# Optimization experiments

Hardware: AMD Instinct MI355X
Metric: run time of the kernel (lower is better)

## Reference

```python
import jax, jax.numpy as jnp
import numpy as np

GROUPS = 32
HEADS = 8
EPS = 1e-5


def setup_inputs() -> dict:
    key = jax.random.key(0)
    k1, k2 = jax.random.split(key)
    B, C, H, W = 8, 512, 32, 32
    x = jax.random.normal(k1, (B, C, H, W), dtype=jnp.float32)
    gn_weight = jnp.ones((C,), dtype=jnp.float32)
    gn_bias = jnp.zeros((C,), dtype=jnp.float32)
    w1 = jax.random.normal(k2, (3 * C, C, 1), dtype=jnp.float32) * (C ** -0.5)
    b1 = jnp.zeros((3 * C,), dtype=jnp.float32)
    return {"x": x, "gn_weight": gn_weight, "gn_bias": gn_bias, "w1": w1, "b1": b1}


def reference(x, gn_weight, gn_bias, w1, b1):
    B, C, H, W = x.shape
    T = H * W
    ch = C // HEADS
    # GroupNorm over (C/G, H, W) per group
    xg = x.reshape(B, GROUPS, -1)
    mu = jnp.mean(xg, axis=-1, keepdims=True)
    var = jnp.var(xg, axis=-1, keepdims=True)
    xn = ((xg - mu) * jax.lax.rsqrt(var + EPS)).reshape(B, C, T)
    xn = xn * gn_weight[:, None] + gn_bias[:, None]
    # 1x1 Conv1d -> QKV: [B, 3C, T]
    qkv = jnp.einsum('oc,bct->bot', w1[:, :, 0], xn) + b1[:, None]
    q, k, v = jnp.split(qkv, 3, axis=1)
    q = q.reshape(B, HEADS, ch, T)
    k = k.reshape(B, HEADS, ch, T)
    v = v.reshape(B, HEADS, ch, T)
    scale = ch ** -0.25  # applied to both q and k, per guided-diffusion QKVAttention
    w = jnp.einsum('bhct,bhcs->bhts', q * scale, k * scale)  # [B,H,T,T]
    w = jax.nn.softmax(w, axis=-1)
    a = jnp.einsum('bhts,bhcs->bhct', w, v).reshape(B, C, H, W)
    return a + x
```

## Files before the change

### kernel.cpp

```cpp
#include <hip/hip_runtime.h>
#include <hip/hip_bf16.h>

#define NB 8
#define NC 512
#define NT 1024
#define NHEADS 8
#define NCH 64
#define NGROUPS 32
#define NGC 16

typedef __attribute__((ext_vector_type(4))) unsigned short u16x4;
typedef __attribute__((ext_vector_type(8))) unsigned short u16x8;
typedef __attribute__((ext_vector_type(4))) float f32x4;
typedef __attribute__((ext_vector_type(8))) __bf16 bfv8;

static __device__ __forceinline__ unsigned short f2bf(float f) {
    __bf16 h = (__bf16)f;
    return __builtin_bit_cast(unsigned short, h);
}

static __device__ __forceinline__ f32x4 mfma_bf16(u16x8 a, u16x8 b, f32x4 c) {
    return __builtin_amdgcn_mfma_f32_16x16x32_bf16(
        __builtin_bit_cast(bfv8, a), __builtin_bit_cast(bfv8, b), c, 0, 0, 0);
}

static __device__ __forceinline__ void gl_lds16(const unsigned short* g, unsigned short* l) {
    __builtin_amdgcn_global_load_lds(
        (const __attribute__((address_space(1))) unsigned int*)g,
        (__attribute__((address_space(3))) unsigned int*)l, 16, 0, 0);
}

__global__ __launch_bounds__(512) void k_gn_w1(const float* __restrict__ x,
                                               const float* __restrict__ gw,
                                               const float* __restrict__ gb,
                                               const float* __restrict__ w1,
                                               unsigned short* __restrict__ xnT,
                                               unsigned short* __restrict__ w1b) {
    int tid = threadIdx.x;
    if (blockIdx.x >= 256) {
        int i = ((blockIdx.x - 256) * 512 + tid) * 8;
        f32x4 a = *(const f32x4*)(w1 + i);
        f32x4 b = *(const f32x4*)(w1 + i + 4);
        u16x8 o;
#pragma unroll
        for (int j = 0; j < 4; ++j) { o[j] = f2bf(a[j]); o[4 + j] = f2bf(b[j]); }
        *(u16x8*)(w1b + i) = o;
        return;
    }
    int b = blockIdx.x >> 5, g = blockIdx.x & 31;
    int half = tid >> 8, tl = tid & 255;
    int t4 = tl * 4;
    const float* xb = x + ((size_t)(b * NC + g * NGC + half * 8)) * NT;

    f32x4 vv[8];
    float s = 0.f, ss = 0.f;
#pragma unroll
    for (int cc = 0; cc < 8; ++cc) {
        f32x4 v = *(const f32x4*)(xb + cc * NT + t4);
        vv[cc] = v;
#pragma unroll
        for (int i = 0; i < 4; ++i) { s += v[i]; ss += v[i] * v[i]; }
    }
#pragma unroll
    for (int off = 1; off < 64; off <<= 1) { s += __shfl_xor(s, off); ss += __shfl_xor(ss, off); }
    __shared__ float rs_[8], rss[8];
    int w = tid >> 6;
    if ((tid & 63) == 0) { rs_[w] = s; rss[w] = ss; }
    __syncthreads();
    s = 0.f; ss = 0.f;
#pragma unroll
    for (int i = 0; i < 8; ++i) { s += rs_[i]; ss += rss[i]; }
    float mu  = s * (1.f / 16384.f);
    float var = ss * (1.f / 16384.f) - mu * mu;
    float rstd = rsqrtf(var + 1e-5f);

    float wgt[8], bia[8];
#pragma unroll
    for (int cc = 0; cc < 8; ++cc) {
        float ww = gw[g * NGC + half * 8 + cc] * rstd;
        wgt[cc] = ww;
        bia[cc] = gb[g * NGC + half * 8 + cc] - mu * ww;
    }
#pragma unroll
    for (int i = 0; i < 4; ++i) {
        unsigned short o[8];
#pragma unroll
        for (int cc = 0; cc < 8; ++cc) o[cc] = f2bf(vv[cc][i] * wgt[cc] + bia[cc]);
        unsigned short* dst = xnT + ((size_t)(b * NT + t4 + i)) * NC + g * NGC + half * 8;
        *(u16x8*)dst = *(u16x8*)o;
    }
}

__global__ __launch_bounds__(256) void k_qkv_gemm(const unsigned short* __restrict__ w1b,
                                                  const unsigned short* __restrict__ xnT,
                                                  const float* __restrict__ b1,
                                                  unsigned short* __restrict__ q_t,
                                                  unsigned short* __restrict__ k_t,
                                                  unsigned short* __restrict__ vbuf) {
    __shared__ unsigned short As[2 * 128 * 64];
    __shared__ unsigned short Bs[2 * 128 * 64];
    int bid = blockIdx.x;
    int lbid = (bid & 7) * 96 + (bid >> 3);
    int bb = lbid / 96;
    int rr_ = lbid % 96;
    int tm = rr_ >> 3, tn = rr_ & 7;
    int tid = threadIdx.x;
    int l = tid & 63, w = tid >> 6;
    int wm = w >> 1, wn = w & 1;
    int ll = l & 15, lg = l >> 4;
    int rl = l >> 3, sl = l & 7;
    int ssl = sl ^ rl;

    const unsigned short* Ag = w1b + (size_t)(tm * 128) * NC;
    const unsigned short* Bg = xnT + (size_t)(bb * NT + tn * 128) * NC;

    auto STAGE = [&](int k0, int buf) {
        unsigned short* dA = As + buf * 8192 + w * 32 * 64;
        unsigned short* dB = Bs + buf * 8192 + w * 32 * 64;
#pragma unroll
        for (int i = 0; i < 4; ++i) {
            int row = w * 32 + i * 8 + rl;
            gl_lds16(Ag + (size_t)row * NC + k0 + ssl * 8, dA + i * 512);
            gl_lds16(Bg + (size_t)row * NC + k0 + ssl * 8, dB + i * 512);
        }
    };

    f32x4 acc[4][4] = {};
    STAGE(0, 0);
    __syncthreads();
    int cur = 0;
    for (int ks = 0; ks < 8; ++ks) {
        if (ks < 7) STAGE((ks + 1) * 64, cur ^ 1);
        const char* Ac = (const char*)(As + cur * 8192);
        const char* Bc = (const char*)(Bs + cur * 8192);
#pragma unroll
        for (int kk = 0; kk < 2; ++kk) {
            u16x8 af[4], bf[4];
#pragma unroll
            for (int m = 0; m < 4; ++m) {
                int row = wm * 64 + m * 16 + ll;
                af[m] = *(const u16x8*)(Ac + row * 128 + ((kk * 64 + lg * 16) ^ ((row & 7) << 4)));
            }
#pragma unroll
            for (int n = 0; n < 4; ++n) {
                int row = wn * 64 + n * 16 + ll;
                bf[n] = *(const u16x8*)(Bc + row * 128 + ((kk * 64 + lg * 16) ^ ((row & 7) << 4)));
            }
#pragma unroll
            for (int m = 0; m < 4; ++m)
#pragma unroll
                for (int n = 0; n < 4; ++n)
                    acc[m][n] = mfma_bf16(af[m], bf[n], acc[m][n]);
        }
        __syncthreads();
        cur ^= 1;
    }

    if (tm < 8) {
        int qk = tm >> 2;
        int h = (tm & 3) * 2 + wm;
        float sc = qk ? 1.f : 0.125f * 1.44269504088896f;
        int obase = tm * 128 + wm * 64;
        unsigned short* dst = (qk ? k_t : q_t) + ((size_t)(bb * 8 + h)) * NT * NCH;
#pragma unroll
        for (int m = 0; m < 4; ++m) {
#pragma unroll
            for (int n = 0; n < 4; ++n) {
                int t = tn * 128 + wn * 64 + n * 16 + ll;
                u16x4 pk;
#pragma unroll
                for (int r = 0; r < 4; ++r)
                    pk[r] = f2bf((acc[m][n][r] + b1[obase + m * 16 + lg * 4 + r]) * sc);
                *(u16x4*)(dst + (size_t)t * NCH + m * 16 + lg * 4) = pk;
            }
        }
    } else {
        int vcb = (tm - 8) * 128 + wm * 64;
#pragma unroll
        for (int m = 0; m < 4; ++m)
#pragma unroll
            for (int r = 0; r < 4; ++r) {
                int vc = vcb + m * 16 + lg * 4 + r;
                float bias = b1[1024 + vc];
#pragma unroll
                for (int n = 0; n < 4; ++n) {
                    int t = tn * 128 + wn * 64 + n * 16 + ll;
                    vbuf[(size_t)(bb * NC + vc) * NT + t] = f2bf(acc[m][n][r] + bias);
                }
            }
    }
}

#define SW1B(r) (((r) & 7) << 4)
__global__ __launch_bounds__(256) void k_attn(const unsigned short* __restrict__ q_t,
                                              const unsigned short* __restrict__ k_t,
                                              const unsigned short* __restrict__ vbuf,
                                              const float* __restrict__ x,
                                              float* __restrict__ out) {
    __shared__ unsigned char smem[49152];
    unsigned short* sK = (unsigned short*)smem;
    unsigned short* sV = (unsigned short*)(smem + 16384);
    unsigned short* sP = (unsigned short*)(smem + 32768);

    int lbid = ((blockIdx.x & 7) << 6) | (blockIdx.x >> 3);
    int b  = lbid >> 6;
    int h  = (lbid >> 3) & 7;
    int qt = lbid & 7;
    int t0 = qt * 128;

    int tid = threadIdx.x;
    int l = tid & 63, w = tid >> 6;
    int ll = l & 15, lg = l >> 4;
    int rl = l >> 3, sl = l & 7;
    int ssl = sl ^ rl;

    const unsigned short* Qg = q_t + ((size_t)((b * 8 + h) * NT + t0 + w * 32)) * NCH;
    const unsigned short* Kg = k_t + ((size_t)(b * 8 + h)) * NT * NCH;
    const unsigned short* Vg = vbuf + ((size_t)(b * NC + h * NCH)) * NT;

    u16x8 aq[2][2];
#pragma unroll
    for (int m = 0; m < 2; ++m)
#pragma unroll
        for (int kk = 0; kk < 2; ++kk)
            aq[m][kk] = *(const u16x8*)(Qg + (m * 16 + ll) * NCH + kk * 32 + lg * 8);

    f32x4 acc_o[2][4] = {};
    float rs[2] = {};

    auto STAGE = [&](int s0, int buf) {
        unsigned short* dK = sK + buf * 4096 + w * 1024;
        unsigned short* dV = sV + buf * 4096 + w * 1024;
#pragma unroll
        for (int i = 0; i < 2; ++i) {
            int row = w * 16 + i * 8 + rl;
            gl_lds16(Kg + (size_t)(s0 + row) * NCH + ssl * 8, dK + i * 512);
            gl_lds16(Vg + (size_t)row * NT + s0 + ssl * 8, dV + i * 512);
        }
    };

    STAGE(0, 0);
    __syncthreads();

    char* sPw = (char*)(sP + w * 2048);
    int cur = 0;
    for (int tile = 0; tile < 16; ++tile) {
        if (tile < 15) STAGE((tile + 1) * 64, cur ^ 1);
        const char* Kc = (const char*)(sK + cur * 4096);
        const char* Vc = (const char*)(sV + cur * 4096);

        f32x4 sc_[2][4];
#pragma unroll
        for (int j = 0; j < 4; ++j) {
            int row = j * 16 + ll;
            int sw = SW1B(row);
            u16x8 b0 = *(const u16x8*)(Kc + row * 128 + ((lg * 16) ^ sw));
            u16x8 b1v = *(const u16x8*)(Kc + row * 128 + ((64 + lg * 16) ^ sw));
            f32x4 z = {0.f, 0.f, 0.f, 0.f};
            sc_[0][j] = mfma_bf16(b1v, aq[0][1], mfma_bf16(b0, aq[0][0], z));
            sc_[1][j] = mfma_bf16(b1v, aq[1][1], mfma_bf16(b0, aq[1][0], z));
        }

#pragma unroll
        for (int m = 0; m < 2; ++m) {
            int t = m * 16 + ll;
            int sw = (t & 7) << 4;
#pragma unroll
            for (int j = 0; j < 4; ++j) {
                float p0 = __builtin_amdgcn_exp2f(sc_[m][j][0]);
                float p1 = __builtin_amdgcn_exp2f(sc_[m][j][1]);
                float p2 = __builtin_amdgcn_exp2f(sc_[m][j][2]);
                float p3 = __builtin_amdgcn_exp2f(sc_[m][j][3]);
                rs[m] += (p0 + p1) + (p2 + p3);
                u16x4 pk = {f2bf(p0), f2bf(p1), f2bf(p2), f2bf(p3)};
                *(u16x4*)(sPw + t * 128 + ((j * 32 + lg * 8) ^ sw)) = pk;
            }
        }

        u16x8 ap[2][2];
#pragma unroll
        for (int m = 0; m < 2; ++m) {
            int t = m * 16 + ll;
            int sw = (t & 7) << 4;
#pragma unroll
            for (int kk = 0; kk < 2; ++kk)
                ap[m][kk] = *(const u16x8*)(sPw + t * 128 + ((kk * 64 + lg * 16) ^ sw));
        }
#pragma unroll
        for (int n = 0; n < 4; ++n) {
            int row = n * 16 + ll;
            int sw = SW1B(row);
#pragma unroll
            for (int kk = 0; kk < 2; ++kk) {
                u16x8 bv = *(const u16x8*)(Vc + row * 128 + ((kk * 64 + lg * 16) ^ sw));
                acc_o[0][n] = mfma_bf16(ap[0][kk], bv, acc_o[0][n]);
                acc_o[1][n] = mfma_bf16(ap[1][kk], bv, acc_o[1][n]);
            }
        }
        __syncthreads();
        cur ^= 1;
    }

    float rinv[2][4];
#pragma unroll
    for (int m = 0; m < 2; ++m) {
        float s = rs[m];
        s += __shfl_xor(s, 16);
        s += __shfl_xor(s, 32);
#pragma unroll
        for (int r = 0; r < 4; ++r)
            rinv[m][r] = 1.f / __shfl(s, (l & 48) + lg * 4 + r);
    }

    char* sO = (char*)(smem + w * 8192);
#pragma unroll
    for (int m = 0; m < 2; ++m)
#pragma unroll
        for (int n = 0; n < 4; ++n) {
            int c = n * 16 + ll;
            f32x4 o4;
#pragma unroll
            for (int r = 0; r < 4; ++r) o4[r] = acc_o[m][n][r] * rinv[m][r];
            *(f32x4*)(sO + c * 128 + ((m * 64 + lg * 16) ^ SW1B(c))) = o4;
        }
#pragma unroll
    for (int i2 = 0; i2 < 8; ++i2) {
        int c = i2 * 8 + rl;
        f32x4 o4 = *(const f32x4*)(sO + c * 128 + ((sl * 16) ^ SW1B(c)));
        size_t gidx = ((size_t)(b * NC + h * NCH + c)) * NT + t0 + w * 32 + sl * 4;
        f32x4 xv = *(const f32x4*)(x + gidx);
#pragma unroll
        for (int q = 0; q < 4; ++q) o4[q] += xv[q];
        *(f32x4*)(out + gidx) = o4;
    }
}

extern "C" void kernel_launch(void* const* d_in, const int* in_sizes, int n_in,
                              void* d_out, int out_size, void* d_ws, size_t ws_size,
                              hipStream_t stream) {
    (void)in_sizes; (void)n_in; (void)out_size; (void)ws_size;
    const float* x  = (const float*)d_in[0];
    const float* gw = (const float*)d_in[1];
    const float* gb = (const float*)d_in[2];
    const float* w1 = (const float*)d_in[3];
    const float* b1 = (const float*)d_in[4];
    float* out = (float*)d_out;

    char* ws = (char*)d_ws;
    unsigned short* w1b  = (unsigned short*)(ws);
    unsigned short* xnT  = (unsigned short*)(ws + (size_t)(2u << 20));
    unsigned short* q_t  = (unsigned short*)(ws + (size_t)(11u << 20));
    unsigned short* k_t  = (unsigned short*)(ws + (size_t)(20u << 20));
    unsigned short* vbuf = (unsigned short*)(ws + (size_t)(29u << 20));

    k_gn_w1<<<dim3(448), dim3(512), 0, stream>>>(x, gw, gb, w1, xnT, w1b);
    k_qkv_gemm<<<dim3(768), dim3(256), 0, stream>>>(w1b, xnT, b1, q_t, k_t, vbuf);
    k_attn<<<dim3(512), dim3(256), 0, stream>>>(q_t, k_t, vbuf, x, out);
}
```

Before: 67.82 us.

## Halve QKV GEMM K-tile and load V directly from global in attention

The QKV GEMM now stages 32-wide K slices instead of 64, halving its LDS footprint and changing the swizzle to fit the smaller 64-byte rows. This doubles the number of pipeline steps and barriers. The attention kernel stops staging V through LDS: each wave reads its V fragments straight from global memory every tile, cutting shared memory from 48KB to 32KB to allow more resident blocks. The cost is that every wave re-reads V from global/L2 without LDS sharing, and those loads are not prefetched ahead of use.

Result: slower. 79.02 us (+16.5%).

```diff
diff --git a/kernel.cpp b/kernel.cpp
--- a/kernel.cpp
+++ b/kernel.cpp
@@ -97,8 +97,8 @@
                                                   unsigned short* __restrict__ q_t,
                                                   unsigned short* __restrict__ k_t,
                                                   unsigned short* __restrict__ vbuf) {
-    __shared__ unsigned short As[2 * 128 * 64];
-    __shared__ unsigned short Bs[2 * 128 * 64];
+    __shared__ unsigned short As[2 * 128 * 32];
+    __shared__ unsigned short Bs[2 * 128 * 32];
     int bid = blockIdx.x;
     int lbid = (bid & 7) * 96 + (bid >> 3);
     int bb = lbid / 96;
@@ -108,20 +108,21 @@
     int l = tid & 63, w = tid >> 6;
     int wm = w >> 1, wn = w & 1;
     int ll = l & 15, lg = l >> 4;
-    int rl = l >> 3, sl = l & 7;
-    int ssl = sl ^ rl;
 
     const unsigned short* Ag = w1b + (size_t)(tm * 128) * NC;
     const unsigned short* Bg = xnT + (size_t)(bb * NT + tn * 128) * NC;
 
+    int srow = l >> 2;
+    int sslot = (l & 3) ^ ((l >> 3) & 3);
+
     auto STAGE = [&](int k0, int buf) {
-        unsigned short* dA = As + buf * 8192 + w * 32 * 64;
-        unsigned short* dB = Bs + buf * 8192 + w * 32 * 64;
-#pragma unroll
-        for (int i = 0; i < 4; ++i) {
-            int row = w * 32 + i * 8 + rl;
-            gl_lds16(Ag + (size_t)row * NC + k0 + ssl * 8, dA + i * 512);
-            gl_lds16(Bg + (size_t)row * NC + k0 + ssl * 8, dB + i * 512);
+        unsigned short* dA = As + buf * 4096 + w * 1024;
+        unsigned short* dB = Bs + buf * 4096 + w * 1024;
+#pragma unroll
+        for (int i = 0; i < 2; ++i) {
+            int row = w * 32 + i * 16 + srow;
+            gl_lds16(Ag + (size_t)row * NC + k0 + sslot * 8, dA + i * 512);
+            gl_lds16(Bg + (size_t)row * NC + k0 + sslot * 8, dB + i * 512);
         }
     };
 
@@ -129,29 +130,27 @@
     STAGE(0, 0);
     __syncthreads();
     int cur = 0;
-    for (int ks = 0; ks < 8; ++ks) {
-        if (ks < 7) STAGE((ks + 1) * 64, cur ^ 1);
-        const char* Ac = (const char*)(As + cur * 8192);
-        const char* Bc = (const char*)(Bs + cur * 8192);
-#pragma unroll
-        for (int kk = 0; kk < 2; ++kk) {
-            u16x8 af[4], bf[4];
-#pragma unroll
-            for (int m = 0; m < 4; ++m) {
-                int row = wm * 64 + m * 16 + ll;
-                af[m] = *(const u16x8*)(Ac + row * 128 + ((kk * 64 + lg * 16) ^ ((row & 7) << 4)));
-            }
-#pragma unroll
-            for (int n = 0; n < 4; ++n) {
-                int row = wn * 64 + n * 16 + ll;
-                bf[n] = *(const u16x8*)(Bc + row * 128 + ((kk * 64 + lg * 16) ^ ((row & 7) << 4)));
-            }
-#pragma unroll
-            for (int m = 0; m < 4; ++m)
-#pragma unroll
-                for (int n = 0; n < 4; ++n)
-                    acc[m][n] = mfma_bf16(af[m], bf[n], acc[m][n]);
-        }
+    int rsw = (ll >> 1) & 3;
+    for (int ks = 0; ks < 16; ++ks) {
+        if (ks < 15) STAGE((ks + 1) * 32, cur ^ 1);
+        const char* Ac = (const char*)(As + cur * 4096);
+        const char* Bc = (const char*)(Bs + cur * 4096);
+        u16x8 af[4], bf[4];
+#pragma unroll
+        for (int m = 0; m < 4; ++m) {
+            int row = wm * 64 + m * 16 + ll;
+            af[m] = *(const u16x8*)(Ac + row * 64 + ((lg ^ rsw) * 16));
+        }
+#pragma unroll
+        for (int n = 0; n < 4; ++n) {
+            int row = wn * 64 + n * 16 + ll;
+            bf[n] = *(const u16x8*)(Bc + row * 64 + ((lg ^ rsw) * 16));
+        }
+#pragma unroll
+        for (int m = 0; m < 4; ++m)
+#pragma unroll
+            for (int n = 0; n < 4; ++n)
+                acc[m][n] = mfma_bf16(af[m], bf[n], acc[m][n]);
         __syncthreads();
         cur ^= 1;
     }
@@ -197,10 +196,9 @@
                                               const unsigned short* __restrict__ vbuf,
                                               const float* __restrict__ x,
                                               float* __restrict__ out) {
-    __shared__ unsigned char smem[49152];
+    __shared__ unsigned char smem[32768];
     unsigned short* sK = (unsigned short*)smem;
-    unsigned short* sV = (unsigned short*)(smem + 16384);
-    unsigned short* sP = (unsigned short*)(smem + 32768);
+    unsigned short* sP = (unsigned short*)(smem + 16384);
 
     int lbid = ((blockIdx.x & 7) << 6) | (blockIdx.x >> 3);
     int b  = lbid >> 6;
@@ -230,12 +228,10 @@
 
     auto STAGE = [&](int s0, int buf) {
         unsigned short* dK = sK + buf * 4096 + w * 1024;
-        unsigned short* dV = sV + buf * 4096 + w * 1024;
 #pragma unroll
         for (int i = 0; i < 2; ++i) {
             int row = w * 16 + i * 8 + rl;
             gl_lds16(Kg + (size_t)(s0 + row) * NCH + ssl * 8, dK + i * 512);
-            gl_lds16(Vg + (size_t)row * NT + s0 + ssl * 8, dV + i * 512);
         }
     };
 
@@ -247,7 +243,14 @@
     for (int tile = 0; tile < 16; ++tile) {
         if (tile < 15) STAGE((tile + 1) * 64, cur ^ 1);
         const char* Kc = (const char*)(sK + cur * 4096);
-        const char* Vc = (const char*)(sV + cur * 4096);
+        const unsigned short* Vt = Vg + tile * 64;
+
+        u16x8 bv[4][2];
+#pragma unroll
+        for (int n = 0; n < 4; ++n)
+#pragma unroll
+            for (int kk = 0; kk < 2; ++kk)
+                bv[n][kk] = *(const u16x8*)(Vt + (size_t)(n * 16 + ll) * NT + kk * 32 + lg * 8);
 
         f32x4 sc_[2][4];
 #pragma unroll
@@ -287,16 +290,12 @@
                 ap[m][kk] = *(const u16x8*)(sPw + t * 128 + ((kk * 64 + lg * 16) ^ sw));
         }
 #pragma unroll
-        for (int n = 0; n < 4; ++n) {
-            int row = n * 16 + ll;
-            int sw = SW1B(row);
+        for (int n = 0; n < 4; ++n)
 #pragma unroll
             for (int kk = 0; kk < 2; ++kk) {
-                u16x8 bv = *(const u16x8*)(Vc + row * 128 + ((kk * 64 + lg * 16) ^ sw));
-                acc_o[0][n] = mfma_bf16(ap[0][kk], bv, acc_o[0][n]);
-                acc_o[1][n] = mfma_bf16(ap[1][kk], bv, acc_o[1][n]);
+                acc_o[0][n] = mfma_bf16(ap[0][kk], bv[n][kk], acc_o[0][n]);
+                acc_o[1][n] = mfma_bf16(ap[1][kk], bv[n][kk], acc_o[1][n]);
             }
-        }
         __syncthreads();
         cur ^= 1;
     }
```
